# Kernel optimization log

Measured on AMD Instinct MI355X. Metric: run time of the kernel, lower is better.

## Reference

```python
import jax, jax.numpy as jnp
import numpy as np
from jax import lax

B, T, IN, H, NC = 512, 512, 128, 256, 10
GRID_SIZE, SPLINE_ORDER = 5, 3


def _grid(in_f):
    h = 2.0 / GRID_SIZE
    pts = jnp.arange(-SPLINE_ORDER, GRID_SIZE + SPLINE_ORDER + 1, dtype=jnp.float32) * h - 1.0
    return jnp.broadcast_to(pts, (in_f, pts.shape[0]))


def _b_splines(x, grid):
    # x: (B, in); grid: (in, GRID_SIZE + 2*SPLINE_ORDER + 1)
    xg = x[..., None]
    b = ((xg >= grid[:, :-1]) & (xg < grid[:, 1:])).astype(x.dtype)
    for k in range(1, SPLINE_ORDER + 1):
        b = ((xg - grid[:, :-(k + 1)]) / (grid[:, k:-1] - grid[:, :-(k + 1)]) * b[..., :-1]
             + (grid[:, k + 1:] - xg) / (grid[:, k + 1:] - grid[:, 1:-k]) * b[..., 1:])
    return b  # (B, in, GRID_SIZE + SPLINE_ORDER)


def _kan_linear(x, base_w, spline_w, scaler):
    g = _grid(x.shape[-1])
    base = jax.nn.silu(x) @ base_w.T
    spline = jnp.einsum('bik,oik->bo', _b_splines(x, g), spline_w * scaler[..., None])
    return base + spline


def _gru_cell(x, h, wih, whh, bih, bhh):
    gi = x @ wih.T + bih
    gh = h @ whh.T + bhh
    ir, iz, inn = jnp.split(gi, 3, axis=-1)
    hr, hz, hn = jnp.split(gh, 3, axis=-1)
    r = jax.nn.sigmoid(ir + hr)
    z = jax.nn.sigmoid(iz + hz)
    n = jnp.tanh(inn + r * hn)
    return (1.0 - z) * n + z * h


def _lstm_single(x, wih, whh, bih, bhh):
    # single-timestep LSTM with zero initial (h, c); gate order i,f,g,o
    h0 = jnp.zeros((x.shape[0], whh.shape[1]), x.dtype)
    g = x @ wih.T + h0 @ whh.T + bih + bhh
    i, f, gg, o = jnp.split(g, 4, axis=-1)
    c = jax.nn.sigmoid(i) * jnp.tanh(gg)
    return jax.nn.sigmoid(o) * jnp.tanh(c)


def setup_inputs() -> dict:
    keys = iter(jax.random.split(jax.random.key(0), 64))
    def w(*shape):
        return jax.random.normal(next(keys), shape, jnp.float32) * 0.1
    d = {}
    d['x'] = jax.random.normal(next(keys), (B, T, IN), jnp.float32)
    d['gru0_wih'] = w(3 * H, IN); d['gru0_whh'] = w(3 * H, H)
    d['gru0_bih'] = w(3 * H); d['gru0_bhh'] = w(3 * H)
    d['gru1_wih'] = w(3 * H, H); d['gru1_whh'] = w(3 * H, H)
    d['gru1_bih'] = w(3 * H); d['gru1_bhh'] = w(3 * H)
    for suf in ['0', '0r', '1', '1r']:
        d['lw_ih' + suf] = w(512, 256); d['lw_hh' + suf] = w(512, 128)
        d['lb_ih' + suf] = w(512); d['lb_hh' + suf] = w(512)
    d['kan1_base'] = w(64, 256); d['kan1_spline'] = w(64, 256, GRID_SIZE + SPLINE_ORDER); d['kan1_scaler'] = w(64, 256)
    d['kan2_base'] = w(NC, 64); d['kan2_spline'] = w(NC, 64, GRID_SIZE + SPLINE_ORDER); d['kan2_scaler'] = w(NC, 64)
    return d


def reference(x, gru0_wih, gru0_whh, gru0_bih, gru0_bhh, gru1_wih, gru1_whh, gru1_bih, gru1_bhh,
              lw_ih0, lw_hh0, lb_ih0, lb_hh0, lw_ih0r, lw_hh0r, lb_ih0r, lb_hh0r,
              lw_ih1, lw_hh1, lb_ih1, lb_hh1, lw_ih1r, lw_hh1r, lb_ih1r, lb_hh1r,
              kan1_base, kan1_spline, kan1_scaler, kan2_base, kan2_spline, kan2_scaler):
    bsz = x.shape[0]
    h_init = (jnp.zeros((bsz, H), x.dtype), jnp.zeros((bsz, H), x.dtype))

    def step(carry, xt):
        h0, h1 = carry
        h0 = _gru_cell(xt, h0, gru0_wih, gru0_whh, gru0_bih, gru0_bhh)
        h1 = _gru_cell(h0, h1, gru1_wih, gru1_whh, gru1_bih, gru1_bhh)
        return (h0, h1), None

    (h0, h1), _ = lax.scan(step, h_init, jnp.swapaxes(x, 0, 1))  # time-major scan
    s = h1  # last layer final hidden, seq_len-1 single step for LSTM
    o0 = jnp.concatenate([_lstm_single(s, lw_ih0, lw_hh0, lb_ih0, lb_hh0),
                          _lstm_single(s, lw_ih0r, lw_hh0r, lb_ih0r, lb_hh0r)], axis=-1)
    o1 = jnp.concatenate([_lstm_single(o0, lw_ih1, lw_hh1, lb_ih1, lb_hh1),
                          _lstm_single(o0, lw_ih1r, lw_hh1r, lb_ih1r, lb_hh1r)], axis=-1)
    z = _kan_linear(o1, kan1_base, kan1_spline, kan1_scaler)
    return _kan_linear(z, kan2_base, kan2_spline, kan2_scaler)
```

## Files before the change

kernel.cpp:

```cpp
#include <hip/hip_runtime.h>
#include <stdint.h>


constexpr int B_  = 512;
constexpr int T_  = 512;
constexpr int IN_ = 128;
constexpr int H_  = 256;
constexpr int GR_ = 32;
constexpr int PL_ = GR_ * 2 * 4096;
constexpr int TCp = 64;
constexpr int NCp = 8;

typedef __attribute__((ext_vector_type(8))) short bf16x8;
typedef __attribute__((ext_vector_type(4))) float f32x4;

#define MFMA16(a, b, c) __builtin_amdgcn_mfma_f32_16x16x32_bf16((a), (b), (c), 0, 0, 0)

__device__ __forceinline__ float bf2f(unsigned short u){
    union { unsigned int i; float f; } v; v.i = ((unsigned int)u) << 16; return v.f;
}
__device__ __forceinline__ unsigned short f2bf(float f){
    union { float f; unsigned int i; } v; v.f = f;
    return (unsigned short)((v.i + 0x7FFFu + ((v.i >> 16) & 1u)) >> 16);
}
__device__ __forceinline__ unsigned int cvtpk(float a, float b){
    unsigned int r;
    asm("v_cvt_pk_bf16_f32 %0, %1, %2" : "=v"(r) : "v"(a), "v"(b));
    return r;
}
__device__ __forceinline__ unsigned long long pk4(float a, float b, float c, float d){
    const unsigned int lo = cvtpk(a, b), hi = cvtpk(c, d);
    return (unsigned long long)lo | ((unsigned long long)hi << 32);
}
__device__ __forceinline__ float sig_(float x){
    return __builtin_amdgcn_rcpf(1.0f + __expf(-x));
}
__device__ __forceinline__ float tanh_(float x){
    return 1.0f - 2.0f * __builtin_amdgcn_rcpf(1.0f + __expf(2.0f * x));
}
__device__ __forceinline__ bf16x8 ldb8g(const unsigned short* p){ return *(const bf16x8*)p; }

union U64x2 { unsigned long long q[2]; bf16x8 v; };

__device__ __forceinline__ void gl2lds16(const void* g, void* l){
    __builtin_amdgcn_global_load_lds(
        (const __attribute__((address_space(1))) unsigned int*)g,
        (__attribute__((address_space(3))) unsigned int*)l, 16, 0, 0);
}

__global__ void srt_detect(const unsigned int* __restrict__ xw, unsigned int* __restrict__ flag){
    int cnt = 0;
    for (int i = threadIdx.x; i < 1024; i += 64){
        const unsigned int lo = xw[i] & 0xFFFFu;
        const int e = (int)((lo >> 7) & 0xFFu);
        if (e >= 100 && e <= 140) cnt++;
    }
    #pragma unroll
    for (int o = 32; o > 0; o >>= 1) cnt += __shfl_down(cnt, o);
    if (threadIdx.x == 0) *flag = (cnt > 614) ? 1u : 0u;
}

struct ConvTab { const void* src[26]; int n[26]; int off[26]; };

__global__ __launch_bounds__(256) void srt_conv(ConvTab ct, unsigned short* __restrict__ wb,
                                                const unsigned int* __restrict__ flag){
    const bool isb = (*flag != 0);
    const int gsz = gridDim.x * blockDim.x;
    const int gid = blockIdx.x * blockDim.x + threadIdx.x;
    for (int j = 0; j < 26; ++j){
        const int n = ct.n[j];
        unsigned short* o = wb + ct.off[j];
        if (isb){
            const unsigned short* s = (const unsigned short*)ct.src[j];
            for (int i = gid; i < n; i += gsz) o[i] = s[i];
        } else {
            const float* s = (const float*)ct.src[j];
            for (int i = gid; i < n; i += gsz) o[i] = f2bf(s[i]);
        }
    }
}

__global__ __launch_bounds__(256) void srt_prep(
    float* __restrict__ h0s, float* __restrict__ h1s,
    float* __restrict__ bias0, float* __restrict__ bias1,
    const unsigned short* __restrict__ b0ih, const unsigned short* __restrict__ b0hh,
    const unsigned short* __restrict__ b1ih, const unsigned short* __restrict__ b1hh,
    unsigned int* __restrict__ seq)
{
    const int gid = blockIdx.x * blockDim.x + threadIdx.x;
    h0s[gid] = 0.f;
    h1s[gid] = 0.f;
    if (gid < 768){
        bias0[gid] = bf2f(b0ih[gid]) + (gid < 512 ? bf2f(b0hh[gid]) : 0.f);
        bias1[gid] = bf2f(b1ih[gid]) + (gid < 512 ? bf2f(b1hh[gid]) : 0.f);
    }
    if (gid < 1024) seq[gid] = 0u;
}

__device__ void seq_dev(unsigned short* shm,
    const unsigned short* __restrict__ gi,
    const unsigned short* __restrict__ whh,
    const unsigned short* __restrict__ bhh,
    float* __restrict__ hstate,
    unsigned short* __restrict__ h_all,
    const int TC, const int bg)
{
    unsigned short* wnL   = shm;
    unsigned short* hbufB = shm + 32768;
    unsigned short* gibB  = shm + 32768 + 8192;

    const int tid  = threadIdx.x;
    const int lane = tid & 63;
    const int wv   = tid >> 6;
    const int l15  = lane & 15;
    const int quad = lane >> 4;
    const int m0   = bg * 16;
    const int swz  = (l15 & 7) << 4;

    bf16x8 wr[5][8];
    #pragma unroll
    for (int fi = 0; fi < 6; ++fi){
        const int u = fi >> 1, ii = fi & 1;
        const unsigned short* wp =
            whh + (size_t)(u * 256 + wv * 32 + ii * 16 + l15) * 256 + quad * 8;
        if (fi < 5){
            #pragma unroll
            for (int kc = 0; kc < 8; ++kc) wr[fi][kc] = ldb8g(wp + kc * 32);
        } else {
            #pragma unroll
            for (int kc = 0; kc < 8; ++kc)
                *(bf16x8*)&wnL[((wv * 8 + kc) << 9) + lane * 8] = ldb8g(wp + kc * 32);
        }
    }

    f32x4 bn0[2];
    #pragma unroll
    for (int ii = 0; ii < 2; ++ii)
        #pragma unroll
        for (int j = 0; j < 4; ++j)
            bn0[ii][j] = bf2f(bhh[512 + wv * 32 + ii * 16 + quad * 4 + j]);

    f32x4 hr[2];
    #pragma unroll
    for (int ii = 0; ii < 2; ++ii)
        hr[ii] = *(const f32x4*)&hstate[(size_t)(m0 + l15) * 256 + wv * 32 + ii * 16 + quad * 4];

    const unsigned short* gpp[3]; int gdl[3];
    #pragma unroll
    for (int i = 0; i < 3; ++i){
        const int g_  = i * 512 + tid;
        const int row = g_ / 96;
        const int cg  = g_ - row * 96;
        gpp[i] = gi + ((size_t)m0 + row) * 768 + ((cg ^ (row & 7)) << 3);
        gdl[i] = g_ * 8;
    }

    #pragma unroll
    for (int ii = 0; ii < 2; ++ii){
        const unsigned long long pk = pk4(hr[ii][0], hr[ii][1], hr[ii][2], hr[ii][3]);
        *(unsigned long long*)((char*)hbufB + l15 * 512 +
            ((wv * 64 + ii * 32 + quad * 8) ^ swz)) = pk;
    }
    #pragma unroll
    for (int i = 0; i < 3; ++i) gl2lds16(gpp[i], &gibB[gdl[i]]);
    __syncthreads();

    #pragma unroll 1
    for (int t = 0; t < TC; ++t){
        const int par = t & 1;
        unsigned short* hb_cur = hbufB + par * 4096;
        unsigned short* hb_nxt = hbufB + (par ^ 1) * 4096;
        unsigned short* gb_cur = gibB + par * 12288;
        unsigned short* gb_nxt = gibB + (par ^ 1) * 12288;

        if (t + 1 < TC){
            const size_t toff = (size_t)(t + 1) * (512 * 768);
            #pragma unroll
            for (int i = 0; i < 3; ++i) gl2lds16(gpp[i] + toff, &gb_nxt[gdl[i]]);
        }

        f32x4 aR0 = {0,0,0,0}, aR1 = {0,0,0,0}, aZ0 = {0,0,0,0}, aZ1 = {0,0,0,0};
        f32x4 aN0 = bn0[0], aN1 = bn0[1];
        __builtin_amdgcn_s_setprio(1);
        #pragma unroll
        for (int kc = 0; kc < 8; ++kc){
            const bf16x8 hb = *(const bf16x8*)((const char*)hb_cur +
                l15 * 512 + ((kc * 64 + quad * 16) ^ swz));
            const bf16x8 w5 = *(const bf16x8*)&wnL[((wv * 8 + kc) << 9) + lane * 8];
            aR0 = MFMA16(wr[0][kc], hb, aR0);
            aR1 = MFMA16(wr[1][kc], hb, aR1);
            aZ0 = MFMA16(wr[2][kc], hb, aZ0);
            aZ1 = MFMA16(wr[3][kc], hb, aZ1);
            aN0 = MFMA16(wr[4][kc], hb, aN0);
            aN1 = MFMA16(w5,        hb, aN1);
        }
        __builtin_amdgcn_s_setprio(0);

        const char* gbase = (const char*)gb_cur + l15 * 1536;
        #pragma unroll
        for (int ii = 0; ii < 2; ++ii){
            const int cb = wv * 64 + ii * 32 + quad * 8;
            const unsigned long long qr = *(const unsigned long long*)(gbase + ((       cb) ^ swz));
            const unsigned long long qz = *(const unsigned long long*)(gbase + ((512  + cb) ^ swz));
            const unsigned long long qn = *(const unsigned long long*)(gbase + ((1024 + cb) ^ swz));
            const f32x4 aR = ii ? aR1 : aR0;
            const f32x4 aZ = ii ? aZ1 : aZ0;
            const f32x4 aN = ii ? aN1 : aN0;
            #pragma unroll
            for (int j = 0; j < 4; ++j){
                const float rr = sig_(aR[j] + bf2f((unsigned short)(qr >> (16 * j))));
                const float zz = sig_(aZ[j] + bf2f((unsigned short)(qz >> (16 * j))));
                const float nn = tanh_(bf2f((unsigned short)(qn >> (16 * j))) + rr * aN[j]);
                hr[ii][j] = (1.0f - zz) * nn + zz * hr[ii][j];
            }
        }

        #pragma unroll
        for (int ii = 0; ii < 2; ++ii){
            const unsigned long long pk = pk4(hr[ii][0], hr[ii][1], hr[ii][2], hr[ii][3]);
            *(unsigned long long*)((char*)hb_nxt + l15 * 512 +
                ((wv * 64 + ii * 32 + quad * 8) ^ swz)) = pk;
            if (h_all)
                *(unsigned long long*)(h_all + ((size_t)t * 512 + m0 + l15) * 256 +
                    wv * 32 + ii * 16 + quad * 4) = pk;
        }

        __syncthreads();
    }

    #pragma unroll
    for (int ii = 0; ii < 2; ++ii)
        *(f32x4*)&hstate[(size_t)(m0 + l15) * 256 + wv * 32 + ii * 16 + quad * 4] = hr[ii];
}

template<int K, bool XS>
__device__ void gemm_dev(unsigned short* shm, const void* Asrc, const bool isb,
                         const int t0, const unsigned short* __restrict__ W,
                         const float* __restrict__ bias,
                         unsigned short* __restrict__ C, const int mb)
{
    unsigned short* Ares = shm;
    unsigned short* Wbuf = shm + 32768;

    const int tid = threadIdx.x;
    const int lane = tid & 63, wv = tid >> 6;
    const int l15 = lane & 15, quad = lane >> 4;
    const int rh = wv & 1, fq = wv >> 1;

    constexpr int GPT = K / 32;
    constexpr int GPR = K / 8;

    if (!XS || isb){
        #pragma unroll
        for (int i = 0; i < GPT; ++i){
            const int g_ = i * 512 + tid;
            const int row = g_ / GPR, cg = g_ % GPR;
            size_t src;
            if (XS){
                const int r = mb * 128 + row;
                const int b = r & 511, tt = r >> 9;
                src = ((size_t)b * 512 + (t0 + tt)) * 128 + ((cg ^ (row & 7)) << 3);
            } else {
                src = (size_t)(mb * 128 + row) * K + ((cg ^ (row & 7)) << 3);
            }
            gl2lds16((const unsigned short*)Asrc + src, &Ares[g_ * 8]);
        }
    } else {
        #pragma unroll
        for (int i = 0; i < GPT; ++i){
            const int g_ = i * 512 + tid;
            const int row = g_ / GPR, cg = g_ % GPR;
            const int r = mb * 128 + row;
            const int b = r & 511, tt = r >> 9;
            const float* p = (const float*)Asrc + ((size_t)b * 512 + (t0 + tt)) * 128 + cg * 8;
            const float4 f0 = *(const float4*)p;
            const float4 f1 = *(const float4*)(p + 4);
            uint4 u;
            u.x = cvtpk(f0.x, f0.y); u.y = cvtpk(f0.z, f0.w);
            u.z = cvtpk(f1.x, f1.y); u.w = cvtpk(f1.z, f1.w);
            *(uint4*)&Ares[(row * GPR + (cg ^ (row & 7))) * 8] = u;
        }
    }

    for (int Nb = 0; Nb < 6; ++Nb){
        f32x4 acc[4][2];
        #pragma unroll
        for (int mi = 0; mi < 4; ++mi){ acc[mi][0] = (f32x4){0,0,0,0}; acc[mi][1] = (f32x4){0,0,0,0}; }

        for (int k0 = 0; k0 < K; k0 += 64){
            __syncthreads();
            #pragma unroll
            for (int i = 0; i < 2; ++i){
                const int g_ = i * 512 + tid;
                const int row = g_ >> 3, cg = g_ & 7;
                gl2lds16(W + (size_t)(Nb * 128 + row) * K + k0 + ((cg ^ (row & 7)) << 3),
                         &Wbuf[g_ * 8]);
            }
            __syncthreads();

            #pragma unroll
            for (int kc = 0; kc < 2; ++kc){
                bf16x8 wf[2], af[4];
                #pragma unroll
                for (int ni = 0; ni < 2; ++ni){
                    const int rf = fq * 32 + ni * 16 + l15;
                    wf[ni] = *(const bf16x8*)((const char*)Wbuf +
                        rf * 128 + (((kc * 4 + quad) ^ (rf & 7)) << 4));
                }
                #pragma unroll
                for (int mi = 0; mi < 4; ++mi){
                    const int ra = rh * 64 + mi * 16 + l15;
                    af[mi] = *(const bf16x8*)((const char*)Ares +
                        ra * (2 * K) + ((((k0 >> 3) + kc * 4 + quad) ^ (ra & 7)) << 4));
                }
                #pragma unroll
                for (int mi = 0; mi < 4; ++mi){
                    acc[mi][0] = MFMA16(wf[0], af[mi], acc[mi][0]);
                    acc[mi][1] = MFMA16(wf[1], af[mi], acc[mi][1]);
                }
            }
        }

        float bs[2][4];
        #pragma unroll
        for (int ni = 0; ni < 2; ++ni)
            #pragma unroll
            for (int j = 0; j < 4; ++j)
                bs[ni][j] = bias[Nb * 128 + fq * 32 + ni * 16 + quad * 4 + j];
        #pragma unroll
        for (int mi = 0; mi < 4; ++mi)
            #pragma unroll
            for (int ni = 0; ni < 2; ++ni){
                const unsigned int lo = cvtpk(acc[mi][ni][0] + bs[ni][0],
                                              acc[mi][ni][1] + bs[ni][1]);
                const unsigned int hi = cvtpk(acc[mi][ni][2] + bs[ni][2],
                                              acc[mi][ni][3] + bs[ni][3]);
                const int row = mb * 128 + rh * 64 + mi * 16 + l15;
                const int col = Nb * 128 + fq * 32 + ni * 16 + quad * 4;
                uint2 st; st.x = lo; st.y = hi;
                *(uint2*)(C + (size_t)row * 768 + col) = st;
            }
    }
}

struct PA {
    const void* xv;
    const unsigned int* flag;
    const unsigned short *w0ih, *w0hh, *b0hh, *w1ih, *w1hh, *b1hh;
    const float *bias0, *bias1;
    float *h0s, *h1s;
    unsigned short *gi0a, *gi0b, *haa, *hab, *gi1a, *gi1b;
    int p;
};

__global__ __launch_bounds__(512, 1) void srt_phase(PA a){
    __shared__ __align__(16) unsigned short shm[65536];
    const int bid = blockIdx.x;
    const int p = a.p;

    if (bid < 32){
        const int c = p - 1; if (c < 0 || c >= NCp) return;
        seq_dev(shm, (c & 1) ? a.gi0b : a.gi0a, a.w0hh, a.b0hh, a.h0s,
                (c & 1) ? a.hab : a.haa, TCp, bid);
    } else if (bid < 64){
        const int c = p - 3; if (c < 0 || c >= NCp) return;
        seq_dev(shm, (c & 1) ? a.gi1b : a.gi1a, a.w1hh, a.b1hh, a.h1s,
                nullptr, TCp, bid - 32);
    } else if (bid < 320){
        const int c = p; if (c >= NCp) return;
        const bool isb = (*a.flag != 0);
        gemm_dev<128, true>(shm, a.xv, isb, c * TCp, a.w0ih, a.bias0,
                            (c & 1) ? a.gi0b : a.gi0a, bid - 64);
    } else {
        const int c = p - 2; if (c < 0 || c >= NCp) return;
        gemm_dev<256, false>(shm, (c & 1) ? a.hab : a.haa, true, 0, a.w1ih, a.bias1,
                             (c & 1) ? a.gi1b : a.gi1a, bid - 320);
    }
}

__global__ __launch_bounds__(256, 1) void srt_gru(
    const void* __restrict__ xv,
    const unsigned short* __restrict__ w0ih,
    const unsigned short* __restrict__ w0hh,
    const unsigned short* __restrict__ b0ih,
    const unsigned short* __restrict__ b0hh,
    const unsigned short* __restrict__ w1ih,
    const unsigned short* __restrict__ w1hh,
    const unsigned short* __restrict__ b1ih,
    const unsigned short* __restrict__ b1hh,
    float* __restrict__ s_out,
    const unsigned int* __restrict__ flagp,
    unsigned int* __restrict__ seq,
    unsigned short* __restrict__ hb)
{
    __shared__ __align__(16) unsigned short w0hhL[4 * 24 * 512];

    const bool isb = (*flagp != 0);
    const int tid  = threadIdx.x;
    const int lane = tid & 63;
    const int wv   = tid >> 6;
    const int l15  = lane & 15;
    const int quad = lane >> 4;
    const int q    = blockIdx.x >> 5;
    const int g    = blockIdx.x & 31;
    const int m0   = g * 16;
    const int c    = q * 64 + wv * 16 + l15;

    bf16x8 w0ihr[3][4];
    #pragma unroll
    for (int u = 0; u < 3; ++u)
        #pragma unroll
        for (int kc = 0; kc < 4; ++kc)
            w0ihr[u][kc] = ldb8g(w0ih + (u * 256 + c) * IN_ + kc * 32 + quad * 8);

    bf16x8 w1ihr[3][8], w1hhr[3][8];
    #pragma unroll
    for (int u = 0; u < 3; ++u)
        #pragma unroll
        for (int kc = 0; kc < 8; ++kc){
            w1ihr[u][kc] = ldb8g(w1ih + (u * 256 + c) * H_ + kc * 32 + quad * 8);
            w1hhr[u][kc] = ldb8g(w1hh + (u * 256 + c) * H_ + kc * 32 + quad * 8);
        }

    const int wl = wv * 12288 + lane * 8;
    #pragma unroll
    for (int u = 0; u < 3; ++u)
        #pragma unroll
        for (int kc = 0; kc < 8; ++kc){
            const bf16x8 f = ldb8g(w0hh + (u * 256 + c) * H_ + kc * 32 + quad * 8);
            *(bf16x8*)&w0hhL[wl + (u * 8 + kc) * 512] = f;
        }

    const float brz0a = bf2f(b0ih[c])       + bf2f(b0hh[c]);
    const float brz0b = bf2f(b0ih[256 + c]) + bf2f(b0hh[256 + c]);
    const float bni0v = bf2f(b0ih[512 + c]);
    const float bnh0v = bf2f(b0hh[512 + c]);
    const float brz1a = bf2f(b1ih[c])       + bf2f(b1hh[c]);
    const float brz1b = bf2f(b1ih[256 + c]) + bf2f(b1hh[256 + c]);
    const float bni1v = bf2f(b1ih[512 + c]);
    const float bnh1v = bf2f(b1hh[512 + c]);
    __syncthreads();

    float h0r[4] = {0.f, 0.f, 0.f, 0.f};
    float h1r[4] = {0.f, 0.f, 0.f, 0.f};

    const size_t xrow = (size_t)(m0 + l15) * (T_ * IN_) + quad * 8;
    const unsigned short* pxb = (const unsigned short*)xv + xrow;
    const float*          pxf = (const float*)xv + xrow;

    unsigned int* sq = seq + g * 32;
    const int wr_row[4] = {(quad * 4 + 0) * 256 + c, (quad * 4 + 1) * 256 + c,
                           (quad * 4 + 2) * 256 + c, (quad * 4 + 3) * 256 + c};

    const f32x4 z4 = {0.f, 0.f, 0.f, 0.f};
    bf16x8 h0A[8], h1A[8];
    #pragma unroll
    for (int kc = 0; kc < 8; ++kc){
        h0A[kc] = (bf16x8)(short)0;
        h1A[kc] = (bf16x8)(short)0;
    }

    #pragma unroll 1
    for (int t = 0; t < T_; ++t){
        const int par = t & 1;
        const unsigned int tgt = 4u * (unsigned)(t + 1);
        unsigned short* plane = hb + par * PL_ + g * (2 * 4096);

        #pragma unroll
        for (int j = 0; j < 4; ++j)
            __hip_atomic_store(&plane[4096 + wr_row[j]], f2bf(h1r[j]),
                               __ATOMIC_RELAXED, __HIP_MEMORY_SCOPE_AGENT);

        bf16x8 ax[4];
        if (isb){
            #pragma unroll
            for (int kc = 0; kc < 4; ++kc) ax[kc] = ldb8g(pxb + t * IN_ + kc * 32);
        } else {
            #pragma unroll
            for (int kc = 0; kc < 4; ++kc){
                const float* p = pxf + t * IN_ + kc * 32;
                const float4 f0 = *(const float4*)p;
                const float4 f1 = *(const float4*)(p + 4);
                bf16x8 a;
                a[0] = (short)f2bf(f0.x); a[1] = (short)f2bf(f0.y);
                a[2] = (short)f2bf(f0.z); a[3] = (short)f2bf(f0.w);
                a[4] = (short)f2bf(f1.x); a[5] = (short)f2bf(f1.y);
                a[6] = (short)f2bf(f1.z); a[7] = (short)f2bf(f1.w);
                ax[kc] = a;
            }
        }

        f32x4 Tr = z4, Tz = z4, Tni = z4, Tnh = z4;
        #pragma unroll
        for (int kc = 0; kc < 4; ++kc){
            Tr  = MFMA16(ax[kc], w0ihr[0][kc], Tr);
            Tz  = MFMA16(ax[kc], w0ihr[1][kc], Tz);
            Tni = MFMA16(ax[kc], w0ihr[2][kc], Tni);
        }
        #pragma unroll
        for (int kc = 0; kc < 8; ++kc){
            const bf16x8 a = h0A[kc];
            Tr  = MFMA16(a, *(const bf16x8*)&w0hhL[wl + (0 * 8 + kc) * 512], Tr);
            Tz  = MFMA16(a, *(const bf16x8*)&w0hhL[wl + (1 * 8 + kc) * 512], Tz);
            Tnh = MFMA16(a, *(const bf16x8*)&w0hhL[wl + (2 * 8 + kc) * 512], Tnh);
        }
        #pragma unroll
        for (int j = 0; j < 4; ++j){
            const float rr = sig_(Tr[j] + brz0a);
            const float zz = sig_(Tz[j] + brz0b);
            const float nn = tanh_(Tni[j] + bni0v + rr * (Tnh[j] + bnh0v));
            h0r[j] = (1.0f - zz) * nn + zz * h0r[j];
        }

        #pragma unroll
        for (int j = 0; j < 4; ++j)
            __hip_atomic_store(&plane[wr_row[j]], f2bf(h0r[j]),
                               __ATOMIC_RELAXED, __HIP_MEMORY_SCOPE_AGENT);

        __syncthreads();
        if (tid == 0)
            __hip_atomic_fetch_add(sq, 1u, __ATOMIC_RELAXED, __HIP_MEMORY_SCOPE_AGENT);
        if (lane == 0){
            while (__hip_atomic_load(sq, __ATOMIC_RELAXED, __HIP_MEMORY_SCOPE_AGENT) < tgt)
                __builtin_amdgcn_s_sleep(1);
        }
        __atomic_signal_fence(__ATOMIC_ACQ_REL);

        {
            const unsigned short* r0 = plane + l15 * 256 + quad * 8;
            #pragma unroll
            for (int kc = 0; kc < 8; ++kc){
                U64x2 u0, u1;
                u0.q[0] = __hip_atomic_load((const unsigned long long*)(r0 + kc * 32),
                                            __ATOMIC_RELAXED, __HIP_MEMORY_SCOPE_AGENT);
                u0.q[1] = __hip_atomic_load((const unsigned long long*)(r0 + kc * 32 + 4),
                                            __ATOMIC_RELAXED, __HIP_MEMORY_SCOPE_AGENT);
                u1.q[0] = __hip_atomic_load((const unsigned long long*)(r0 + 4096 + kc * 32),
                                            __ATOMIC_RELAXED, __HIP_MEMORY_SCOPE_AGENT);
                u1.q[1] = __hip_atomic_load((const unsigned long long*)(r0 + 4096 + kc * 32 + 4),
                                            __ATOMIC_RELAXED, __HIP_MEMORY_SCOPE_AGENT);
                h0A[kc] = u0.v;
                h1A[kc] = u1.v;
            }
        }

        Tr = z4; Tz = z4; Tni = z4; Tnh = z4;
        #pragma unroll
        for (int kc = 0; kc < 8; ++kc){
            const bf16x8 a0 = h0A[kc];
            const bf16x8 a1 = h1A[kc];
            Tr  = MFMA16(a0, w1ihr[0][kc], Tr);
            Tr  = MFMA16(a1, w1hhr[0][kc], Tr);
            Tz  = MFMA16(a0, w1ihr[1][kc], Tz);
            Tz  = MFMA16(a1, w1hhr[1][kc], Tz);
            Tni = MFMA16(a0, w1ihr[2][kc], Tni);
            Tnh = MFMA16(a1, w1hhr[2][kc], Tnh);
        }
        #pragma unroll
        for (int j = 0; j < 4; ++j){
            const float rr = sig_(Tr[j] + brz1a);
            const float zz = sig_(Tz[j] + brz1b);
            const float nn = tanh_(Tni[j] + bni1v + rr * (Tnh[j] + bnh1v));
            h1r[j] = (1.0f - zz) * nn + zz * h1r[j];
        }
    }

    #pragma unroll
    for (int j = 0; j < 4; ++j)
        s_out[(size_t)(m0 + quad * 4 + j) * H_ + c] = h1r[j];
}

__device__ __forceinline__ float knot_(int p){ return (float)(p - 3) * 0.4f - 1.0f; }

__device__ __forceinline__ void bspline8(float xv, float* bb8){
    float bb[11];
    #pragma unroll
    for (int p = 0; p < 11; ++p)
        bb[p] = (xv >= knot_(p) && xv < knot_(p + 1)) ? 1.f : 0.f;
    #pragma unroll
    for (int k = 1; k <= 3; ++k){
        #pragma unroll
        for (int p = 0; p <= 10 - k; ++p){
            const float tp = knot_(p), tpk = knot_(p + k);
            const float tp1 = knot_(p + 1), tpk1 = knot_(p + k + 1);
            bb[p] = (xv - tp) / (tpk - tp) * bb[p] + (tpk1 - xv) / (tpk1 - tp1) * bb[p + 1];
        }
    }
    #pragma unroll
    for (int j = 0; j < 8; ++j) bb8[j] = bb[j];
}

__device__ __forceinline__ float lstm_unit(const float* sxv, const unsigned short* w,
                                           const unsigned short* bi, const unsigned short* bh,
                                           int uu){
    const unsigned short* wi = w + (size_t)uu * 256;
    const unsigned short* wg = w + (size_t)(256 + uu) * 256;
    const unsigned short* wo = w + (size_t)(384 + uu) * 256;
    float ai = 0.f, ag = 0.f, ao = 0.f;
    for (int k = 0; k < 256; k += 8){
        const bf16x8 vi = ldb8g(wi + k);
        const bf16x8 vg = ldb8g(wg + k);
        const bf16x8 vo = ldb8g(wo + k);
        #pragma unroll
        for (int j = 0; j < 8; ++j){
            const float s = sxv[k + j];
            ai += bf2f((unsigned short)vi[j]) * s;
            ag += bf2f((unsigned short)vg[j]) * s;
            ao += bf2f((unsigned short)vo[j]) * s;
        }
    }
    const float gi = ai + bf2f(bi[uu])       + bf2f(bh[uu]);
    const float gg = ag + bf2f(bi[256 + uu]) + bf2f(bh[256 + uu]);
    const float go = ao + bf2f(bi[384 + uu]) + bf2f(bh[384 + uu]);
    return sig_(go) * tanh_(sig_(gi) * tanh_(gg));
}

__global__ __launch_bounds__(256) void srt_tail(
    const float* __restrict__ in,
    const unsigned short* __restrict__ w0f, const unsigned short* __restrict__ bi0f,
    const unsigned short* __restrict__ bh0f,
    const unsigned short* __restrict__ w0r, const unsigned short* __restrict__ bi0r,
    const unsigned short* __restrict__ bh0r,
    const unsigned short* __restrict__ w1f, const unsigned short* __restrict__ bi1f,
    const unsigned short* __restrict__ bh1f,
    const unsigned short* __restrict__ w1r, const unsigned short* __restrict__ bi1r,
    const unsigned short* __restrict__ bh1r,
    const unsigned short* __restrict__ k1b, const unsigned short* __restrict__ k1s,
    const unsigned short* __restrict__ k1c,
    const unsigned short* __restrict__ k2b, const unsigned short* __restrict__ k2s,
    const unsigned short* __restrict__ k2c,
    void* __restrict__ outp,
    const unsigned int* __restrict__ flagp)
{
    __shared__ float sx[256];
    __shared__ float sy[256];
    __shared__ float sil[256];
    __shared__ float spl[256][8];
    __shared__ float red[64][4];
    __shared__ float sil2[64];
    __shared__ float spl2[64][8];

    const int b = blockIdx.x, tid = threadIdx.x;
    const int dir = tid >> 7, uu = tid & 127;

    sx[tid] = in[b * 256 + tid];
    __syncthreads();

    sy[tid] = lstm_unit(sx, dir ? w0r : w0f, dir ? bi0r : bi0f, dir ? bh0r : bh0f, uu);
    __syncthreads();

    const float o1v = lstm_unit(sy, dir ? w1r : w1f, dir ? bi1r : bi1f, dir ? bh1r : bh1f, uu);

    sil[tid] = o1v * sig_(o1v);
    float bb[8];
    bspline8(o1v, bb);
    #pragma unroll
    for (int j = 0; j < 8; ++j) spl[tid][j] = bb[j];
    __syncthreads();

    const int o = tid >> 2, qq = tid & 3;
    float acc = 0.f;
    for (int k = qq * 64; k < qq * 64 + 64; ++k){
        acc += sil[k] * bf2f(k1b[o * 256 + k]);
        float t = 0.f;
        #pragma unroll
        for (int j = 0; j < 8; ++j) t += spl[k][j] * bf2f(k1s[(o * 256 + k) * 8 + j]);
        acc += t * bf2f(k1c[o * 256 + k]);
    }
    red[o][qq] = acc;
    __syncthreads();

    if (tid < 64){
        const float zv = red[tid][0] + red[tid][1] + red[tid][2] + red[tid][3];
        sil2[tid] = zv * sig_(zv);
        float b2[8];
        bspline8(zv, b2);
        #pragma unroll
        for (int j = 0; j < 8; ++j) spl2[tid][j] = b2[j];
    }
    __syncthreads();

    if (tid < 10){
        float a2 = 0.f;
        for (int k = 0; k < 64; ++k){
            a2 += sil2[k] * bf2f(k2b[tid * 64 + k]);
            float t = 0.f;
            #pragma unroll
            for (int j = 0; j < 8; ++j) t += spl2[k][j] * bf2f(k2s[(tid * 64 + k) * 8 + j]);
            a2 += t * bf2f(k2c[tid * 64 + k]);
        }
        if (*flagp) ((unsigned short*)outp)[b * 10 + tid] = f2bf(a2);
        else        ((float*)outp)[b * 10 + tid] = a2;
    }
}

extern "C" void kernel_launch(void* const* d_in, const int* in_sizes, int n_in,
                              void* d_out, int out_size, void* d_ws, size_t ws_size,
                              hipStream_t stream)
{
    unsigned int* flag = (unsigned int*)d_ws;
    float* s = (float*)((char*)d_ws + 16);
    unsigned short* wb = (unsigned short*)(s + 512 * 256);

    const int idxs[26] = {1,2,3,4,5,6,7,8, 9,11,12, 13,15,16, 17,19,20, 21,23,24,
                          25,26,27, 28,29,30};
    ConvTab ct;
    int off = 0;
    int offs[26];
    for (int j = 0; j < 26; ++j){
        ct.src[j] = d_in[idxs[j]];
        ct.n[j]   = in_sizes[idxs[j]];
        ct.off[j] = off;
        offs[j]   = off;
        off += in_sizes[idxs[j]];
    }
    uintptr_t p = (uintptr_t)(wb + off);
    p = (p + 255) & ~(uintptr_t)255;
    unsigned int* seq = (unsigned int*)p;
    unsigned short* hb = (unsigned short*)(seq + 1024);
    p = (uintptr_t)(hb + 2 * 32 * 2 * 4096);
    p = (p + 255) & ~(uintptr_t)255;
    float* h0s   = (float*)p;
    float* bias0 = h0s + 512 * 256;
    float* bias1 = bias0 + 768;
    p = (uintptr_t)(bias1 + 768);
    p = (p + 255) & ~(uintptr_t)255;
    char* dyn = (char*)p;
    const size_t used = (size_t)(dyn - (char*)d_ws);

    const size_t slab_gi = (size_t)TCp * 512 * 768;
    const size_t slab_ha = (size_t)TCp * 512 * 256;
    const size_t pipe_need = used + (4 * slab_gi + 2 * slab_ha) * sizeof(unsigned short);
    const bool pipe_ok = pipe_need <= ws_size;

    const unsigned short *w0ih = wb + offs[0],  *w0hh = wb + offs[1];
    const unsigned short *b0ih = wb + offs[2],  *b0hh = wb + offs[3];
    const unsigned short *w1ih = wb + offs[4],  *w1hh = wb + offs[5];
    const unsigned short *b1ih = wb + offs[6],  *b1hh = wb + offs[7];
    const unsigned short *lwih0  = wb + offs[8],  *lbih0  = wb + offs[9],  *lbhh0  = wb + offs[10];
    const unsigned short *lwih0r = wb + offs[11], *lbih0r = wb + offs[12], *lbhh0r = wb + offs[13];
    const unsigned short *lwih1  = wb + offs[14], *lbih1  = wb + offs[15], *lbhh1  = wb + offs[16];
    const unsigned short *lwih1r = wb + offs[17], *lbih1r = wb + offs[18], *lbhh1r = wb + offs[19];
    const unsigned short *k1b = wb + offs[20], *k1s = wb + offs[21], *k1c = wb + offs[22];
    const unsigned short *k2b = wb + offs[23], *k2s = wb + offs[24], *k2c = wb + offs[25];

    srt_detect<<<1, 64, 0, stream>>>((const unsigned int*)d_in[0], flag);
    srt_conv<<<1024, 256, 0, stream>>>(ct, wb, flag);
    srt_prep<<<512, 256, 0, stream>>>(h0s, s, bias0, bias1, b0ih, b0hh, b1ih, b1hh, seq);

    if (pipe_ok){
        unsigned short* gi0a = (unsigned short*)dyn;
        unsigned short* gi0b = gi0a + slab_gi;
        unsigned short* haa  = gi0b + slab_gi;
        unsigned short* hab  = haa + slab_ha;
        unsigned short* gi1a = hab + slab_ha;
        unsigned short* gi1b = gi1a + slab_gi;

        PA a;
        a.xv = d_in[0]; a.flag = flag;
        a.w0ih = w0ih; a.w0hh = w0hh; a.b0hh = b0hh;
        a.w1ih = w1ih; a.w1hh = w1hh; a.b1hh = b1hh;
        a.bias0 = bias0; a.bias1 = bias1;
        a.h0s = h0s; a.h1s = s;
        a.gi0a = gi0a; a.gi0b = gi0b; a.haa = haa; a.hab = hab;
        a.gi1a = gi1a; a.gi1b = gi1b;
        for (int ph = 0; ph <= NCp + 2; ++ph){
            a.p = ph;
            srt_phase<<<576, 512, 0, stream>>>(a);
        }
    } else {
        srt_gru<<<128, 256, 0, stream>>>(d_in[0], w0ih, w0hh, b0ih, b0hh,
                                         w1ih, w1hh, b1ih, b1hh, s, flag, seq, hb);
    }

    srt_tail<<<512, 256, 0, stream>>>(s,
        lwih0, lbih0, lbhh0, lwih0r, lbih0r, lbhh0r,
        lwih1, lbih1, lbhh1, lwih1r, lbih1r, lbhh1r,
        k1b, k1s, k1c, k2b, k2s, k2c, d_out, flag);
}
```

Measured before the change: 1.774 ms.

## Triple-buffer weight tiles in GEMM and split tail kernel across 1024 threads

```diff
diff --git a/kernel.cpp b/kernel.cpp
--- a/kernel.cpp
+++ b/kernel.cpp
@@ -240,7 +240,6 @@
                          unsigned short* __restrict__ C, const int mb)
 {
     unsigned short* Ares = shm;
-    unsigned short* Wbuf = shm + 32768;
 
     const int tid = threadIdx.x;
     const int lane = tid & 63, wv = tid >> 6;
@@ -249,6 +248,8 @@
 
     constexpr int GPT = K / 32;
     constexpr int GPR = K / 8;
+    constexpr int NK  = K / 64;
+    constexpr int NIT = 6 * NK;
 
     if (!XS || isb){
         #pragma unroll
@@ -282,36 +283,55 @@
         }
     }
 
+    auto stageW = [&](int i){
+        const int Nb = i / NK, k0 = (i % NK) * 64;
+        unsigned short* dst = shm + 32768 + (i % 3) * 8192;
+        #pragma unroll
+        for (int j = 0; j < 2; ++j){
+            const int g_ = j * 512 + tid;
+            const int row = g_ >> 3, cg = g_ & 7;
+            gl2lds16(W + (size_t)(Nb * 128 + row) * K + k0 + ((cg ^ (row & 7)) << 3),
+                     &dst[g_ * 8]);
+        }
+    };
+
+    stageW(0);
+    stageW(1);
+    if (XS && !isb) asm volatile("s_waitcnt lgkmcnt(0)" ::: "memory");
+
     for (int Nb = 0; Nb < 6; ++Nb){
         f32x4 acc[4][2];
         #pragma unroll
-        for (int mi = 0; mi < 4; ++mi){ acc[mi][0] = (f32x4){0,0,0,0}; acc[mi][1] = (f32x4){0,0,0,0}; }
-
-        for (int k0 = 0; k0 < K; k0 += 64){
-            __syncthreads();
-            #pragma unroll
-            for (int i = 0; i < 2; ++i){
-                const int g_ = i * 512 + tid;
-                const int row = g_ >> 3, cg = g_ & 7;
-                gl2lds16(W + (size_t)(Nb * 128 + row) * K + k0 + ((cg ^ (row & 7)) << 3),
-                         &Wbuf[g_ * 8]);
-            }
-            __syncthreads();
-
+        for (int mi = 0; mi < 4; ++mi){
+            acc[mi][0] = (f32x4){0,0,0,0};
+            acc[mi][1] = (f32x4){0,0,0,0};
+        }
+
+        #pragma unroll
+        for (int kk = 0; kk < NK; ++kk){
+            const int i = Nb * NK + kk;
+            if (Nb == 0 && kk == 0)      asm volatile("s_waitcnt vmcnt(2)"  ::: "memory");
+            else if (kk == 0)            asm volatile("s_waitcnt vmcnt(10)" ::: "memory");
+            else                         asm volatile("s_waitcnt vmcnt(2)"  ::: "memory");
+            __builtin_amdgcn_s_barrier();
+            __builtin_amdgcn_sched_barrier(0);
+            if (i + 2 < NIT) stageW(i + 2);
+
+            const unsigned short* wbuf = shm + 32768 + (i % 3) * 8192;
             #pragma unroll
             for (int kc = 0; kc < 2; ++kc){
                 bf16x8 wf[2], af[4];
                 #pragma unroll
                 for (int ni = 0; ni < 2; ++ni){
                     const int rf = fq * 32 + ni * 16 + l15;
-                    wf[ni] = *(const bf16x8*)((const char*)Wbuf +
+                    wf[ni] = *(const bf16x8*)((const char*)wbuf +
                         rf * 128 + (((kc * 4 + quad) ^ (rf & 7)) << 4));
                 }
                 #pragma unroll
                 for (int mi = 0; mi < 4; ++mi){
                     const int ra = rh * 64 + mi * 16 + l15;
                     af[mi] = *(const bf16x8*)((const char*)Ares +
-                        ra * (2 * K) + ((((k0 >> 3) + kc * 4 + quad) ^ (ra & 7)) << 4));
+                        ra * (2 * K) + (((kk * 8 + kc * 4 + quad) ^ (ra & 7)) << 4));
                 }
                 #pragma unroll
                 for (int mi = 0; mi < 4; ++mi){
@@ -590,32 +610,28 @@
     for (int j = 0; j < 8; ++j) bb8[j] = bb[j];
 }
 
-__device__ __forceinline__ float lstm_unit(const float* sxv, const unsigned short* w,
-                                           const unsigned short* bi, const unsigned short* bh,
-                                           int uu){
-    const unsigned short* wi = w + (size_t)uu * 256;
-    const unsigned short* wg = w + (size_t)(256 + uu) * 256;
-    const unsigned short* wo = w + (size_t)(384 + uu) * 256;
+__device__ __forceinline__ void lstm_part(const float* sxv, const unsigned short* w,
+                                          int uu, int k0, float* out3){
+    const unsigned short* wi = w + (size_t)uu * 256 + k0;
+    const unsigned short* wg = w + (size_t)(256 + uu) * 256 + k0;
+    const unsigned short* wo = w + (size_t)(384 + uu) * 256 + k0;
     float ai = 0.f, ag = 0.f, ao = 0.f;
-    for (int k = 0; k < 256; k += 8){
+    for (int k = 0; k < 64; k += 8){
         const bf16x8 vi = ldb8g(wi + k);
         const bf16x8 vg = ldb8g(wg + k);
         const bf16x8 vo = ldb8g(wo + k);
         #pragma unroll
         for (int j = 0; j < 8; ++j){
-            const float s = sxv[k + j];
+            const float s = sxv[k0 + k + j];
             ai += bf2f((unsigned short)vi[j]) * s;
             ag += bf2f((unsigned short)vg[j]) * s;
             ao += bf2f((unsigned short)vo[j]) * s;
         }
     }
-    const float gi = ai + bf2f(bi[uu])       + bf2f(bh[uu]);
-    const float gg = ag + bf2f(bi[256 + uu]) + bf2f(bh[256 + uu]);
-    const float go = ao + bf2f(bi[384 + uu]) + bf2f(bh[384 + uu]);
-    return sig_(go) * tanh_(sig_(gi) * tanh_(gg));
-}
-
-__global__ __launch_bounds__(256) void srt_tail(
+    out3[0] = ai; out3[1] = ag; out3[2] = ao;
+}
+
+__global__ __launch_bounds__(1024) void srt_tail(
     const float* __restrict__ in,
     const unsigned short* __restrict__ w0f, const unsigned short* __restrict__ bi0f,
     const unsigned short* __restrict__ bh0f,
@@ -634,44 +650,76 @@
 {
     __shared__ float sx[256];
     __shared__ float sy[256];
+    __shared__ float part[4][256][3];
     __shared__ float sil[256];
     __shared__ float spl[256][8];
-    __shared__ float red[64][4];
+    __shared__ float red16[64][16];
     __shared__ float sil2[64];
     __shared__ float spl2[64][8];
+    __shared__ float red2[10][16];
 
     const int b = blockIdx.x, tid = threadIdx.x;
-    const int dir = tid >> 7, uu = tid & 127;
-
-    sx[tid] = in[b * 256 + tid];
-    __syncthreads();
-
-    sy[tid] = lstm_unit(sx, dir ? w0r : w0f, dir ? bi0r : bi0f, dir ? bh0r : bh0f, uu);
-    __syncthreads();
-
-    const float o1v = lstm_unit(sy, dir ? w1r : w1f, dir ? bi1r : bi1f, dir ? bh1r : bh1f, uu);
-
-    sil[tid] = o1v * sig_(o1v);
-    float bb[8];
-    bspline8(o1v, bb);
-    #pragma unroll
-    for (int j = 0; j < 8; ++j) spl[tid][j] = bb[j];
-    __syncthreads();
-
-    const int o = tid >> 2, qq = tid & 3;
-    float acc = 0.f;
-    for (int k = qq * 64; k < qq * 64 + 64; ++k){
-        acc += sil[k] * bf2f(k1b[o * 256 + k]);
-        float t = 0.f;
-        #pragma unroll
-        for (int j = 0; j < 8; ++j) t += spl[k][j] * bf2f(k1s[(o * 256 + k) * 8 + j]);
-        acc += t * bf2f(k1c[o * 256 + k]);
-    }
-    red[o][qq] = acc;
-    __syncthreads();
-
+    const int qr = tid >> 8, sub = tid & 255;
+    const int dir = sub >> 7, uu = sub & 127;
+
+    if (tid < 256) sx[tid] = in[b * 256 + tid];
+    __syncthreads();
+
+    float p3[3];
+    lstm_part(sx, dir ? w0r : w0f, uu, qr * 64, p3);
+    part[qr][sub][0] = p3[0]; part[qr][sub][1] = p3[1]; part[qr][sub][2] = p3[2];
+    __syncthreads();
+    if (tid < 256){
+        const unsigned short* bi = dir ? bi0r : bi0f;
+        const unsigned short* bh = dir ? bh0r : bh0f;
+        const float ai = part[0][sub][0] + part[1][sub][0] + part[2][sub][0] + part[3][sub][0];
+        const float ag = part[0][sub][1] + part[1][sub][1] + part[2][sub][1] + part[3][sub][1];
+        const float ao = part[0][sub][2] + part[1][sub][2] + part[2][sub][2] + part[3][sub][2];
+        const float gi = ai + bf2f(bi[uu])       + bf2f(bh[uu]);
+        const float gg = ag + bf2f(bi[256 + uu]) + bf2f(bh[256 + uu]);
+        const float go = ao + bf2f(bi[384 + uu]) + bf2f(bh[384 + uu]);
+        sy[sub] = sig_(go) * tanh_(sig_(gi) * tanh_(gg));
+    }
+    __syncthreads();
+
+    lstm_part(sy, dir ? w1r : w1f, uu, qr * 64, p3);
+    part[qr][sub][0] = p3[0]; part[qr][sub][1] = p3[1]; part[qr][sub][2] = p3[2];
+    __syncthreads();
+    if (tid < 256){
+        const unsigned short* bi = dir ? bi1r : bi1f;
+        const unsigned short* bh = dir ? bh1r : bh1f;
+        const float ai = part[0][sub][0] + part[1][sub][0] + part[2][sub][0] + part[3][sub][0];
+        const float ag = part[0][sub][1] + part[1][sub][1] + part[2][sub][1] + part[3][sub][1];
+        const float ao = part[0][sub][2] + part[1][sub][2] + part[2][sub][2] + part[3][sub][2];
+        const float gi = ai + bf2f(bi[uu])       + bf2f(bh[uu]);
+        const float gg = ag + bf2f(bi[256 + uu]) + bf2f(bh[256 + uu]);
+        const float go = ao + bf2f(bi[384 + uu]) + bf2f(bh[384 + uu]);
+        const float o1v = sig_(go) * tanh_(sig_(gi) * tanh_(gg));
+        sil[sub] = o1v * sig_(o1v);
+        float bb[8];
+        bspline8(o1v, bb);
+        #pragma unroll
+        for (int j = 0; j < 8; ++j) spl[sub][j] = bb[j];
+    }
+    __syncthreads();
+
+    {
+        const int o = tid >> 4, q16 = tid & 15;
+        float acc = 0.f;
+        for (int k = q16 * 16; k < q16 * 16 + 16; ++k){
+            acc += sil[k] * bf2f(k1b[o * 256 + k]);
+            float t = 0.f;
+            #pragma unroll
+            for (int j = 0; j < 8; ++j) t += spl[k][j] * bf2f(k1s[(o * 256 + k) * 8 + j]);
+            acc += t * bf2f(k1c[o * 256 + k]);
+        }
+        red16[o][q16] = acc;
+    }
+    __syncthreads();
     if (tid < 64){
-        const float zv = red[tid][0] + red[tid][1] + red[tid][2] + red[tid][3];
+        float zv = 0.f;
+        #pragma unroll
+        for (int i = 0; i < 16; ++i) zv += red16[tid][i];
         sil2[tid] = zv * sig_(zv);
         float b2[8];
         bspline8(zv, b2);
@@ -680,15 +728,23 @@
     }
     __syncthreads();
 
+    if (tid < 160){
+        const int o2 = tid >> 4, q = tid & 15;
+        float a2 = 0.f;
+        for (int k = q * 4; k < q * 4 + 4; ++k){
+            a2 += sil2[k] * bf2f(k2b[o2 * 64 + k]);
+            float t = 0.f;
+            #pragma unroll
+            for (int j = 0; j < 8; ++j) t += spl2[k][j] * bf2f(k2s[(o2 * 64 + k) * 8 + j]);
+            a2 += t * bf2f(k2c[o2 * 64 + k]);
+        }
+        red2[o2][q] = a2;
+    }
+    __syncthreads();
     if (tid < 10){
         float a2 = 0.f;
-        for (int k = 0; k < 64; ++k){
-            a2 += sil2[k] * bf2f(k2b[tid * 64 + k]);
-            float t = 0.f;
-            #pragma unroll
-            for (int j = 0; j < 8; ++j) t += spl2[k][j] * bf2f(k2s[(tid * 64 + k) * 8 + j]);
-            a2 += t * bf2f(k2c[tid * 64 + k]);
-        }
+        #pragma unroll
+        for (int i = 0; i < 16; ++i) a2 += red2[tid][i];
         if (*flagp) ((unsigned short*)outp)[b * 10 + tid] = f2bf(a2);
         else        ((float*)outp)[b * 10 + tid] = a2;
     }
@@ -773,7 +829,7 @@
                                          w1ih, w1hh, b1ih, b1hh, s, flag, seq, hb);
     }
 
-    srt_tail<<<512, 256, 0, stream>>>(s,
+    srt_tail<<<512, 1024, 0, stream>>>(s,
         lwih0, lbih0, lbhh0, lwih0r, lbih0r, lbhh0r,
         lwih1, lbih1, lbhh1, lwih1r, lbih1r, lbhh1r,
         k1b, k1s, k1c, k2b, k2s, k2c, d_out, flag);
```

After: 1.752 ms. No clear change (-1.2%).
